# Performance work log

Measured on AMD Instinct MI355X. Metric: run time of the kernel, lower is better.

Reference implementation:

```python
import jax, jax.numpy as jnp
import numpy as np

B, NPATCH, PDIM, DIM, OUTD = 4, 1024, 768, 512, 512
DIN, DSTATE, DTRANK, KCONV, NBLK = 2 * DIM, 16, DIM // 16, 4, 2


def _ln(x, w, b, eps=1e-5):
    m = jnp.mean(x, -1, keepdims=True)
    v = jnp.var(x, -1, keepdims=True)
    return (x - m) * jax.lax.rsqrt(v + eps) * w + b


def _mamba_block(x, ln_w, ln_b, in_W, conv_w, conv_b, xproj_W, dt_W, dt_b, A_log, Dp, out_W):
    # x: [b, L, dim]
    b, L, _ = x.shape
    xn = _ln(x, ln_w, ln_b)
    xz = xn @ in_W                                # [b, L, 2*DIN]
    u, z = jnp.split(xz, 2, axis=-1)              # each [b, L, DIN]
    # causal depthwise conv over time
    uc = jnp.transpose(u, (0, 2, 1))              # [b, DIN, L]
    uc = jax.lax.conv_general_dilated(
        uc, conv_w[:, None, :], window_strides=(1,), padding=((KCONV - 1, 0),),
        feature_group_count=DIN)
    uc = uc + conv_b[None, :, None]
    u = jax.nn.silu(jnp.transpose(uc, (0, 2, 1)))  # [b, L, DIN]
    x_dbl = u @ xproj_W                            # [b, L, DTRANK+2*DSTATE]
    dt, Bm, Cm = jnp.split(x_dbl, [DTRANK, DTRANK + DSTATE], axis=-1)
    delta = jax.nn.softplus(dt @ dt_W + dt_b)      # [b, L, DIN]
    A = -jnp.exp(A_log)                            # [DIN, DSTATE]
    dA = jnp.exp(delta[..., None] * A)             # [b, L, DIN, DSTATE]
    dBu = delta[..., None] * Bm[:, :, None, :] * u[..., None]  # [b, L, DIN, DSTATE]
    # selective scan over time
    def step(h, inp):
        dA_t, dBu_t, C_t = inp                     # [b,DIN,DSTATE],[b,DIN,DSTATE],[b,DSTATE]
        h = dA_t * h + dBu_t
        y = jnp.einsum('bdn,bn->bd', h, C_t)
        return h, y
    h0 = jnp.zeros((b, DIN, DSTATE), x.dtype)
    _, ys = jax.lax.scan(step, h0, (jnp.swapaxes(dA, 0, 1), jnp.swapaxes(dBu, 0, 1), jnp.swapaxes(Cm, 0, 1)))
    y = jnp.swapaxes(ys, 0, 1) + u * Dp            # [b, L, DIN]
    y = y * jax.nn.silu(z)
    return x + y @ out_W                           # residual


def setup_inputs() -> dict:
    key = jax.random.key(0)
    ks = iter(jax.random.split(key, 40))
    rn = lambda shape, s=0.02: jax.random.normal(next(ks), shape, jnp.float32) * s
    d = {
        'img': jax.random.normal(next(ks), (B, NPATCH, PDIM), jnp.float32),
        'patch_W': rn((PDIM, DIM)), 'patch_b': jnp.zeros((DIM,), jnp.float32),
        'pos_emb': rn((1, NPATCH + 1, DIM), 1.0), 'cls_tok': rn((1, 1, DIM), 1.0),
        'blk_ln_w': jnp.ones((NBLK, DIM)), 'blk_ln_b': jnp.zeros((NBLK, DIM)),
        'blk_in_W': rn((NBLK, DIM, 2 * DIN)),
        'blk_conv_w': rn((NBLK, DIN, KCONV), 0.1), 'blk_conv_b': jnp.zeros((NBLK, DIN)),
        'blk_xproj_W': rn((NBLK, DIN, DTRANK + 2 * DSTATE)),
        'blk_dt_W': rn((NBLK, DTRANK, DIN), 0.1), 'blk_dt_b': jnp.full((NBLK, DIN), -4.0),
        'blk_A_log': jnp.tile(jnp.log(jnp.arange(1, DSTATE + 1, dtype=jnp.float32))[None, None, :], (NBLK, DIN, 1)),
        'blk_D': jnp.ones((NBLK, DIN)),
        'blk_out_W': rn((NBLK, DIN, DIM)),
        'sl1_W': rn((DIM, OUTD)), 'sl1_b': jnp.zeros((OUTD,)),
        'sl1_lnw': jnp.ones((OUTD,)), 'sl1_lnb': jnp.zeros((OUTD,)),
        'sl2_W': rn((OUTD, OUTD)), 'sl2_b': jnp.zeros((OUTD,)),
        'sl2_lnw': jnp.ones((OUTD,)), 'sl2_lnb': jnp.zeros((OUTD,)),
        'lat_lnw': jnp.ones((OUTD,)), 'lat_lnb': jnp.zeros((OUTD,)),
    }
    return d


def reference(img, patch_W, patch_b, pos_emb, cls_tok,
              blk_ln_w, blk_ln_b, blk_in_W, blk_conv_w, blk_conv_b,
              blk_xproj_W, blk_dt_W, blk_dt_b, blk_A_log, blk_D, blk_out_W,
              sl1_W, sl1_b, sl1_lnw, sl1_lnb, sl2_W, sl2_b, sl2_lnw, sl2_lnb,
              lat_lnw, lat_lnb):
    x = img @ patch_W + patch_b                       # [b, n, dim]
    b, n, _ = x.shape
    cls = jnp.broadcast_to(cls_tok, (b, 1, DIM))
    x = jnp.concatenate([cls, x], axis=1) + pos_emb[:, :n + 1]
    for i in range(NBLK):
        x = _mamba_block(x, blk_ln_w[i], blk_ln_b[i], blk_in_W[i], blk_conv_w[i],
                         blk_conv_b[i], blk_xproj_W[i], blk_dt_W[i], blk_dt_b[i],
                         blk_A_log[i], blk_D[i], blk_out_W[i])
    y = jax.nn.gelu(_ln(x @ sl1_W + sl1_b, sl1_lnw, sl1_lnb), approximate=False)
    a = jax.nn.gelu(_ln(y @ sl2_W + sl2_b, sl2_lnw, sl2_lnb), approximate=False)
    z = jax.nn.softmax(a, axis=1)                     # softmax over sequence dim
    pooled = jnp.sum(y * z, axis=1)                   # [b, outdim]
    return _ln(pooled, lat_lnw, lat_lnb)
```

## Files before the change

kernel.cpp:

```cpp
#include <hip/hip_runtime.h>
#include <cstdint>
#include <cstddef>

#define B_     4
#define NPATCH 1024
#define LSEQ   1025
#define PDIM   768
#define DIM    512
#define OUTD   512
#define DIN    1024
#define DSTATE 16
#define DTRANK 32
#define KCONV  4
#define NBLK   2
#define MROWS  (B_*LSEQ)
#define NSEG_SP 17

typedef unsigned short u16;
typedef __attribute__((ext_vector_type(8))) short bf16x8;
typedef __attribute__((ext_vector_type(4))) float f32x4;

__device__ __forceinline__ float sigmoidf_(float x){ return 1.f/(1.f+__expf(-x)); }
__device__ __forceinline__ float geluf_(float x){ return 0.5f*x*(1.f+erff(x*0.70710678118654752f)); }
__device__ __forceinline__ u16 f2bf(float x){
    uint32_t b = __float_as_uint(x);
    b += 0x7FFFu + ((b >> 16) & 1u);
    return (u16)(b >> 16);
}
template<int CTRL>
__device__ __forceinline__ float dppmov(float x){
    return __int_as_float(__builtin_amdgcn_update_dpp(0, __float_as_int(x), CTRL, 0xF, 0xF, true));
}
__device__ __forceinline__ float red16(float p){
    p += dppmov<0xB1>(p);
    p += dppmov<0x4E>(p);
    p += dppmov<0x141>(p);
    p += dppmov<0x140>(p);
    return p;
}
__device__ __forceinline__ void gload16(const void* g, void* l){
    __builtin_amdgcn_global_load_lds((const __attribute__((address_space(1))) void*)g,
                                     (__attribute__((address_space(3))) void*)l, 16, 0, 0);
}

template<int MF>
__global__ __launch_bounds__(256) void gemm_mfma(
    const u16* __restrict__ A, int lda,
    const u16* __restrict__ Wt,
    float* __restrict__ C, int ldc,
    int M, int N, int K,
    const float* __restrict__ bias,
    const float* __restrict__ addsrc,
    int act, u16* __restrict__ bf16out)
{
    __shared__ u16 lsA[MF*32*32];
    __shared__ u16 lsB[128*32];
    const int tid = threadIdx.x;
    const int wid = tid >> 6, lane = tid & 63;
    const int m0 = blockIdx.y * (MF*32), n0 = blockIdx.x * 128;
    const int wm = (wid>>1)*(MF*16), wn = (wid&1)*64;
    f32x4 acc[MF][4] = {};

    const char* Agp = (const char*)(A + (size_t)m0 * lda);
    const char* Bgp = (const char*)(Wt + (size_t)n0 * K);
    const int lrow = lane >> 2;
    const int lcb  = (lane & 3) * 16;

    for (int k0 = 0; k0 < K; k0 += 32) {
        {
            int ra = wid*(MF*8) + lrow;
            gload16(Agp + (size_t)ra*(lda*2) + k0*2 + lcb, &lsA[(wid*(MF*8))*32]);
            if constexpr (MF == 4) {
                gload16(Agp + (size_t)(ra+16)*(lda*2) + k0*2 + lcb, &lsA[(wid*(MF*8)+16)*32]);
            }
        }
        {
            int rb = wid*32 + lrow;
            gload16(Bgp + (size_t)rb*(K*2) + k0*2 + lcb, &lsB[(wid*32)*32]);
            gload16(Bgp + (size_t)(rb+16)*(K*2) + k0*2 + lcb, &lsB[(wid*32+16)*32]);
        }
        __syncthreads();
        bf16x8 af[MF], bfr[4];
        #pragma unroll
        for (int i = 0; i < MF; ++i)
            af[i] = *(const bf16x8*)&lsA[(wm + i*16 + (lane&15))*32 + (lane>>4)*8];
        #pragma unroll
        for (int j = 0; j < 4; ++j)
            bfr[j] = *(const bf16x8*)&lsB[(wn + j*16 + (lane&15))*32 + (lane>>4)*8];
        #pragma unroll
        for (int i = 0; i < MF; ++i)
            #pragma unroll
            for (int j = 0; j < 4; ++j)
                acc[i][j] = __builtin_amdgcn_mfma_f32_16x16x32_bf16(af[i], bfr[j], acc[i][j], 0, 0, 0);
        __syncthreads();
    }
    #pragma unroll
    for (int i = 0; i < MF; ++i) {
        #pragma unroll
        for (int j = 0; j < 4; ++j) {
            int col = n0 + wn + j*16 + (lane & 15);
            float bv = bias ? bias[col] : 0.f;
            #pragma unroll
            for (int r = 0; r < 4; ++r) {
                int row = m0 + wm + i*16 + (lane>>4)*4 + r;
                if (row < M) {
                    float v = acc[i][j][r] + bv;
                    if (addsrc) v += addsrc[(size_t)row*ldc + col];
                    if (act == 1) v = (v > 20.f) ? v : log1pf(__expf(v));
                    C[(size_t)row*ldc + col] = v;
                    if (bf16out) bf16out[(size_t)row*ldc + col] = f2bf(v);
                }
            }
        }
    }
}

__global__ __launch_bounds__(256) void xproj_gemm(
    const float* __restrict__ Au,
    const float* __restrict__ W,
    float* __restrict__ P)
{
    __shared__ float As[16][68];
    __shared__ float Bs[16][68];
    int tid = threadIdx.x;
    int tx = tid & 15, ty = tid >> 4;
    int m0 = blockIdx.x * 64;
    int kbase = blockIdx.y * 256;
    float acc[4][4] = {};
    for (int k0 = kbase; k0 < kbase + 256; k0 += 16) {
        {
            int r  = tid >> 2;
            int kq = (tid & 3) << 2;
            float4 va = make_float4(0.f,0.f,0.f,0.f);
            int gr = m0 + r;
            if (gr < MROWS) va = *reinterpret_cast<const float4*>(Au + (size_t)gr*DIN + k0 + kq);
            As[kq+0][r]=va.x; As[kq+1][r]=va.y; As[kq+2][r]=va.z; As[kq+3][r]=va.w;
        }
        {
            int kk = tid >> 4;
            int nq = (tid & 15) << 2;
            float4 vb = *reinterpret_cast<const float4*>(W + (size_t)(k0+kk)*64 + nq);
            Bs[kk][nq+0]=vb.x; Bs[kk][nq+1]=vb.y; Bs[kk][nq+2]=vb.z; Bs[kk][nq+3]=vb.w;
        }
        __syncthreads();
        #pragma unroll
        for (int k = 0; k < 16; ++k) {
            float a0=As[k][ty*4+0],a1=As[k][ty*4+1],a2=As[k][ty*4+2],a3=As[k][ty*4+3];
            float b0=Bs[k][tx*4+0],b1=Bs[k][tx*4+1],b2=Bs[k][tx*4+2],b3=Bs[k][tx*4+3];
            acc[0][0]=fmaf(a0,b0,acc[0][0]); acc[0][1]=fmaf(a0,b1,acc[0][1]);
            acc[0][2]=fmaf(a0,b2,acc[0][2]); acc[0][3]=fmaf(a0,b3,acc[0][3]);
            acc[1][0]=fmaf(a1,b0,acc[1][0]); acc[1][1]=fmaf(a1,b1,acc[1][1]);
            acc[1][2]=fmaf(a1,b2,acc[1][2]); acc[1][3]=fmaf(a1,b3,acc[1][3]);
            acc[2][0]=fmaf(a2,b0,acc[2][0]); acc[2][1]=fmaf(a2,b1,acc[2][1]);
            acc[2][2]=fmaf(a2,b2,acc[2][2]); acc[2][3]=fmaf(a2,b3,acc[2][3]);
            acc[3][0]=fmaf(a3,b0,acc[3][0]); acc[3][1]=fmaf(a3,b1,acc[3][1]);
            acc[3][2]=fmaf(a3,b2,acc[3][2]); acc[3][3]=fmaf(a3,b3,acc[3][3]);
        }
        __syncthreads();
    }
    float* Pp = P + (size_t)blockIdx.y * (MROWS*64);
    #pragma unroll
    for (int i = 0; i < 4; ++i) {
        int r = m0 + ty*4 + i;
        if (r >= MROWS) continue;
        #pragma unroll
        for (int j = 0; j < 4; ++j)
            Pp[(size_t)r*64 + tx*4 + j] = acc[i][j];
    }
}

__global__ __launch_bounds__(256) void xproj_reduce(
    const float* __restrict__ P, float* __restrict__ xdbl, u16* __restrict__ xdbl_bf)
{
    int idx = blockIdx.x*256 + threadIdx.x;
    float v = P[idx] + P[MROWS*64 + idx] + P[2*MROWS*64 + idx] + P[3*MROWS*64 + idx];
    xdbl[idx] = v;
    xdbl_bf[idx] = f2bf(v);
}

__device__ void tcast(const float* __restrict__ in, u16* __restrict__ outp,
                      int K, int N, int tix)
{
    __shared__ float tl[32][33];
    int ntn = N >> 5;
    int tk = tix / ntn, tn = tix - tk*ntn;
    int tid = threadIdx.x;
    int r = tid >> 3, c0 = (tid & 7) << 2;
    float4 v = *(const float4*)&in[(size_t)(tk*32 + r)*N + tn*32 + c0];
    tl[r][c0+0]=v.x; tl[r][c0+1]=v.y; tl[r][c0+2]=v.z; tl[r][c0+3]=v.w;
    __syncthreads();
    int nn = r, k0 = c0;
    uint32_t w0 = f2bf(tl[k0+0][nn]) | ((uint32_t)f2bf(tl[k0+1][nn]) << 16);
    uint32_t w1 = f2bf(tl[k0+2][nn]) | ((uint32_t)f2bf(tl[k0+3][nn]) << 16);
    uint2 o; o.x = w0; o.y = w1;
    *(uint2*)&outp[(size_t)(tn*32 + nn)*K + tk*32 + k0] = o;
}

__global__ __launch_bounds__(256) void prep_kernel(
    const float* __restrict__ img, const float* __restrict__ pW,
    const float* __restrict__ inW, const float* __restrict__ outW,
    const float* __restrict__ dtW, const float* __restrict__ s1W,
    const float* __restrict__ s2W,
    u16* imgb, u16* pWt, u16* inWt, u16* outWt, u16* dtWt, u16* s1t, u16* s2t)
{
    int b = blockIdx.x;
    if (b < 3072) {
        int idx = b*1024 + threadIdx.x*4;
        float4 v = *(const float4*)&img[idx];
        uint2 o;
        o.x = f2bf(v.x) | ((uint32_t)f2bf(v.y) << 16);
        o.y = f2bf(v.z) | ((uint32_t)f2bf(v.w) << 16);
        *(uint2*)&imgb[idx] = o;
        return;
    }
    b -= 3072;
    if (b < 384)  { tcast(pW, pWt, 768, 512, b); return; }
    b -= 384;
    if (b < 2048) { int blk=b>>10, t=b&1023; tcast(inW + (size_t)blk*512*2048, inWt + (size_t)blk*1048576, 512, 2048, t); return; }
    b -= 2048;
    if (b < 1024) { int blk=b>>9, t=b&511; tcast(outW + (size_t)blk*1024*512, outWt + (size_t)blk*524288, 1024, 512, t); return; }
    b -= 1024;
    if (b < 64)   { int blk=b>>5, t=b&31; tcast(dtW + (size_t)blk*32*1024, dtWt + (size_t)blk*32768, 32, 1024, t); return; }
    b -= 64;
    if (b < 256)  { tcast(s1W, s1t, 512, 512, b); return; }
    b -= 256;
    tcast(s2W, s2t, 512, 512, b);
}

__global__ __launch_bounds__(256) void assemble_x(
    const float* __restrict__ tmp, const float* __restrict__ cls,
    const float* __restrict__ pos, float* __restrict__ x)
{
    int idx = blockIdx.x*256 + threadIdx.x;
    int d = idx & 511;
    int r = idx >> 9;
    int l = r % LSEQ;
    int b = r / LSEQ;
    float v = (l == 0) ? cls[d] : tmp[((size_t)(b*NPATCH + l-1))*DIM + d];
    x[idx] = v + pos[(size_t)l*DIM + d];
}

__global__ __launch_bounds__(256) void ln_act(
    const float* __restrict__ in, const float* __restrict__ gw, const float* __restrict__ gb,
    float* __restrict__ f32out, u16* __restrict__ bf16out, int act)
{
    int row = blockIdx.x;
    const float* p = in + (size_t)row * 512;
    int t = threadIdx.x;
    float v0 = p[t], v1 = p[t + 256];
    float s = v0 + v1, q = v0*v0 + v1*v1;
    #pragma unroll
    for (int o = 32; o; o >>= 1) { s += __shfl_xor(s, o); q += __shfl_xor(q, o); }
    __shared__ float ls[4], lq[4];
    int w = t >> 6;
    if ((t & 63) == 0) { ls[w] = s; lq[w] = q; }
    __syncthreads();
    s = ls[0]+ls[1]+ls[2]+ls[3];
    q = lq[0]+lq[1]+lq[2]+lq[3];
    float mean = s * (1.f/512.f);
    float var  = q * (1.f/512.f) - mean*mean;
    float inv  = rsqrtf(var + 1e-5f);
    float o0 = (v0-mean)*inv*gw[t]     + gb[t];
    float o1 = (v1-mean)*inv*gw[t+256] + gb[t+256];
    if (act == 2) { o0 = geluf_(o0); o1 = geluf_(o1); }
    if (f32out)  { f32out[(size_t)row*512 + t] = o0; f32out[(size_t)row*512 + t + 256] = o1; }
    if (bf16out) { bf16out[(size_t)row*512 + t] = f2bf(o0); bf16out[(size_t)row*512 + t + 256] = f2bf(o1); }
}

__global__ __launch_bounds__(256) void conv_silu(
    const float* __restrict__ xz, const float* __restrict__ cw,
    const float* __restrict__ cb, float* __restrict__ uo)
{
    int idx = blockIdx.x*256 + threadIdx.x;
    int dq = idx & 255;
    int r  = idx >> 8;
    int b = r / LSEQ, l = r - b*LSEQ;
    int d0 = dq << 2;
    float4 w0 = *(const float4*)&cw[(d0+0)*4];
    float4 w1 = *(const float4*)&cw[(d0+1)*4];
    float4 w2 = *(const float4*)&cw[(d0+2)*4];
    float4 w3 = *(const float4*)&cw[(d0+3)*4];
    float4 acc = *(const float4*)&cb[d0];
    const float* wv0 = &w0.x; const float* wv1 = &w1.x;
    const float* wv2 = &w2.x; const float* wv3 = &w3.x;
    #pragma unroll
    for (int k = 0; k < KCONV; ++k) {
        int ls = l - (KCONV-1) + k;
        if (ls >= 0) {
            float4 v = *(const float4*)&xz[((size_t)(b*LSEQ + ls))*2048 + d0];
            acc.x = fmaf(wv0[k], v.x, acc.x);
            acc.y = fmaf(wv1[k], v.y, acc.y);
            acc.z = fmaf(wv2[k], v.z, acc.z);
            acc.w = fmaf(wv3[k], v.w, acc.w);
        }
    }
    acc.x *= sigmoidf_(acc.x);
    acc.y *= sigmoidf_(acc.y);
    acc.z *= sigmoidf_(acc.z);
    acc.w *= sigmoidf_(acc.w);
    *(float4*)&uo[(size_t)r*DIN + d0] = acc;
}

__global__ __launch_bounds__(256) void scan_phase1(
    const float* __restrict__ delta, const float* __restrict__ u,
    const float* __restrict__ xdbl,  const float* __restrict__ A_log,
    float* __restrict__ Aseg, float* __restrict__ Hseg)
{
    const int dg = blockIdx.x, b = blockIdx.y, s = blockIdx.z;
    const int tid = threadIdx.x;
    const int n = tid & 15, dl = tid >> 4;
    const int d0 = dg*16, d = d0 + dl;
    const float Adn = -__expf(A_log[(size_t)d*DSTATE + n]);
    float ap = 1.f, h = 0.f;
    __shared__ float sD[16][16], sU[16][16], sB[16][16];
    const size_t base = (size_t)b*LSEQ + (size_t)s*128;
    for (int c0 = 0; c0 < 128; c0 += 16) {
        __syncthreads();
        {
            int tr = tid >> 4, tc = tid & 15;
            size_t row = base + c0 + tr;
            sD[tr][tc] = delta[row*DIN + d0+tc];
            sU[tr][tc] = u[row*DIN + d0+tc];
            sB[tr][tc] = xdbl[row*64 + DTRANK + tc];
        }
        __syncthreads();
        #pragma unroll
        for (int t = 0; t < 16; ++t) {
            float dv = sD[t][dl], uv = sU[t][dl], Bv = sB[t][n];
            float dA = __expf(dv * Adn);
            ap *= dA;
            h = fmaf(dA, h, dv*uv*Bv);
        }
    }
    int dn = d*DSTATE + n;
    Aseg[((size_t)b*7 + s)*16384 + dn] = ap;
    Hseg[((size_t)b*8 + s)*16384 + dn] = h;
}

__global__ __launch_bounds__(256) void scan_mid(
    float* __restrict__ Hseg, const float* __restrict__ Aseg)
{
    int idx = blockIdx.x*256 + threadIdx.x;
    int b = idx >> 14, dn = idx & 16383;
    float prev = 0.f;
    #pragma unroll
    for (int s = 0; s < 7; ++s) {
        size_t offH = ((size_t)b*8 + s)*16384 + dn;
        float a  = Aseg[((size_t)b*7 + s)*16384 + dn];
        float hs = Hseg[offH];
        Hseg[offH] = prev;
        prev = fmaf(a, prev, hs);
    }
    Hseg[((size_t)b*8 + 7)*16384 + dn] = prev;
}

__global__ __launch_bounds__(256) void scan_phase2(
    const float* __restrict__ delta, const float* __restrict__ u,
    const float* __restrict__ xdbl,  const float* __restrict__ xz,
    const float* __restrict__ A_log, const float* __restrict__ Dp,
    const float* __restrict__ H0, u16* __restrict__ yb)
{
    const int dg = blockIdx.x, b = blockIdx.y, s = blockIdx.z;
    const int tid = threadIdx.x;
    const int n = tid & 15, dl = tid >> 4;
    const int d0 = dg*16, d = d0 + dl;
    const float Adn = -__expf(A_log[(size_t)d*DSTATE + n]);
    const float Dd = Dp[d];
    float h = H0[((size_t)b*8 + s)*16384 + d*DSTATE + n];
    __shared__ float sD[16][16], sU[16][16], sZ[16][16], sB[16][16], sC[16][16];
    __shared__ u16 sY[16][16];
    const size_t base = (size_t)b*LSEQ + (size_t)s*128;
    for (int c0 = 0; c0 < 128; c0 += 16) {
        __syncthreads();
        {
            int tr = tid >> 4, tc = tid & 15;
            size_t row = base + c0 + tr;
            sD[tr][tc] = delta[row*DIN + d0+tc];
            sU[tr][tc] = u[row*DIN + d0+tc];
            sZ[tr][tc] = xz[row*2048 + DIN + d0+tc];
            sB[tr][tc] = xdbl[row*64 + DTRANK + tc];
            sC[tr][tc] = xdbl[row*64 + DTRANK + DSTATE + tc];
        }
        __syncthreads();
        #pragma unroll
        for (int t = 0; t < 16; ++t) {
            float dv = sD[t][dl], uv = sU[t][dl], Bv = sB[t][n], Cv = sC[t][n];
            float dA = __expf(dv * Adn);
            h = fmaf(dA, h, dv*uv*Bv);
            float p = red16(h * Cv);
            if (n == 0) {
                float zv = sZ[t][dl];
                sY[t][dl] = f2bf((p + uv*Dd) * (zv * sigmoidf_(zv)));
            }
        }
        __syncthreads();
        {
            int tr = tid >> 4, tc = tid & 15;
            yb[(base + c0 + tr)*DIN + d0 + tc] = sY[tr][tc];
        }
    }
    if (s == 7) {
        size_t row = (size_t)b*LSEQ + 1024;
        float dv = delta[row*DIN + d];
        float uv = u[row*DIN + d];
        float zv = xz[row*2048 + DIN + d];
        float Bv = xdbl[row*64 + DTRANK + n];
        float Cv = xdbl[row*64 + DTRANK + DSTATE + n];
        float dA = __expf(dv * Adn);
        h = fmaf(dA, h, dv*uv*Bv);
        float p = red16(h * Cv);
        if (n == 0)
            yb[row*DIN + d] = f2bf((p + uv*Dd) * (zv * sigmoidf_(zv)));
    }
}

__global__ __launch_bounds__(256) void softpool_seg(
    const float* __restrict__ a, const float* __restrict__ yh,
    float* __restrict__ pm, float* __restrict__ ps, float* __restrict__ pp)
{
    int b   = blockIdx.y;
    int seg = blockIdx.z;
    int jj = threadIdx.x & 63;
    int j  = blockIdx.x * 64 + jj;
    int li = threadIdx.x >> 6;
    int lbeg = seg * 64;
    int lend = min(lbeg + 64, LSEQ);
    float m = -3.0e38f, s = 0.f, p = 0.f;
    for (int l = lbeg + li; l < lend; l += 4) {
        size_t off = ((size_t)(b*LSEQ + l))*OUTD + j;
        float av = a[off], yv = yh[off];
        float mn = fmaxf(m, av);
        float sc = __expf(m - mn);
        float e  = __expf(av - mn);
        s = s*sc + e;
        p = p*sc + yv*e;
        m = mn;
    }
    __shared__ float sm[4][64], ss[4][64], sp[4][64];
    sm[li][jj] = m; ss[li][jj] = s; sp[li][jj] = p;
    __syncthreads();
    if (li == 0) {
        #pragma unroll
        for (int k2 = 1; k2 < 4; ++k2) {
            float m2 = sm[k2][jj], s2 = ss[k2][jj], p2 = sp[k2][jj];
            float M2 = fmaxf(m, m2);
            float c1 = __expf(m - M2), c2 = __expf(m2 - M2);
            s = s*c1 + s2*c2;
            p = p*c1 + p2*c2;
            m = M2;
        }
        int o = ((seg*B_ + b)*OUTD) + j;
        pm[o] = m; ps[o] = s; pp[o] = p;
    }
}

__global__ __launch_bounds__(256) void softpool_combine(
    const float* __restrict__ pm, const float* __restrict__ ps,
    const float* __restrict__ pp, float* __restrict__ pooled)
{
    int idx = blockIdx.x*256 + threadIdx.x;
    int b = idx >> 9, j = idx & 511;
    float m = -3.0e38f, s = 0.f, p = 0.f;
    #pragma unroll
    for (int seg = 0; seg < NSEG_SP; ++seg) {
        int o = ((seg*B_ + b)*OUTD) + j;
        float m2 = pm[o], s2 = ps[o], p2 = pp[o];
        float M2 = fmaxf(m, m2);
        float c1 = __expf(m - M2), c2 = __expf(m2 - M2);
        s = s*c1 + s2*c2;
        p = p*c1 + p2*c2;
        m = M2;
    }
    pooled[(size_t)b*OUTD + j] = p / s;
}

extern "C" void kernel_launch(void* const* d_in, const int* in_sizes, int n_in,
                              void* d_out, int out_size, void* d_ws, size_t ws_size,
                              hipStream_t stream) {
    const float* img     = (const float*)d_in[0];
    const float* patch_W = (const float*)d_in[1];
    const float* patch_b = (const float*)d_in[2];
    const float* pos_emb = (const float*)d_in[3];
    const float* cls_tok = (const float*)d_in[4];
    const float* ln_w    = (const float*)d_in[5];
    const float* ln_b    = (const float*)d_in[6];
    const float* in_W    = (const float*)d_in[7];
    const float* conv_w  = (const float*)d_in[8];
    const float* conv_b  = (const float*)d_in[9];
    const float* xproj_W = (const float*)d_in[10];
    const float* dt_W    = (const float*)d_in[11];
    const float* dt_b    = (const float*)d_in[12];
    const float* A_log   = (const float*)d_in[13];
    const float* Dp      = (const float*)d_in[14];
    const float* out_W   = (const float*)d_in[15];
    const float* sl1_W   = (const float*)d_in[16];
    const float* sl1_b   = (const float*)d_in[17];
    const float* sl1_lnw = (const float*)d_in[18];
    const float* sl1_lnb = (const float*)d_in[19];
    const float* sl2_W   = (const float*)d_in[20];
    const float* sl2_b   = (const float*)d_in[21];
    const float* sl2_lnw = (const float*)d_in[22];
    const float* sl2_lnb = (const float*)d_in[23];
    const float* lat_lnw = (const float*)d_in[24];
    const float* lat_lnb = (const float*)d_in[25];
    float* out = (float*)d_out;
    float* ws  = (float*)d_ws;

    float* x     = ws + 0;
    float* xz    = ws + 2099200;
    float* u     = ws + 10496000;
    float* xdbl  = ws + 14694400;
    float* delta = ws + 14956800;
    u16* ub      = (u16*)(ws + 19155200);
    u16* regA    = ub + 0;
    u16* regB    = ub + 4325376;
    u16* xdbl_bf = ub + 6488064;
    u16* pWt     = ub + 6758400;
    u16* inWt    = ub + 7151616;
    u16* outWt   = ub + 9248768;
    u16* dtWt    = ub + 10297344;
    u16* s1t     = ub + 10362880;
    u16* s2t     = ub + 10625024;

    float* yh     = xz;
    float* t2     = xz + 2099200;
    float* a      = u;
    float* pooled = xdbl;
    float* spm    = xdbl + 8192;
    float* sps    = spm + 34816;
    float* spp    = sps + 34816;
    float* t1     = delta;
    float* segH   = (float*)regB;
    float* segA   = segH + 524288;
    float* xprojP = delta;

    prep_kernel<<<7104, 256, 0, stream>>>(img, patch_W, in_W, out_W, dt_W, sl1_W, sl2_W,
                                          regA, pWt, inWt, outWt, dtWt, s1t, s2t);

    gemm_mfma<2><<<dim3(512/128, 4096/64), 256, 0, stream>>>(
        regA, PDIM, pWt, delta, DIM, 4096, DIM, PDIM, patch_b, nullptr, 0, nullptr);
    assemble_x<<<(MROWS*DIM)/256, 256, 0, stream>>>(delta, cls_tok, pos_emb, x);

    for (int i = 0; i < NBLK; ++i) {
        ln_act<<<MROWS, 256, 0, stream>>>(x, ln_w + i*DIM, ln_b + i*DIM,
                                          nullptr, regB, 0);
        gemm_mfma<4><<<dim3(2048/128, 33), 256, 0, stream>>>(
            regB, DIM, inWt + (size_t)i*1048576, xz, 2*DIN,
            MROWS, 2*DIN, DIM, nullptr, nullptr, 0, nullptr);
        conv_silu<<<MROWS, 256, 0, stream>>>(
            xz, conv_w + i*DIN*KCONV, conv_b + i*DIN, u);
        xproj_gemm<<<dim3(65, 4), 256, 0, stream>>>(
            u, xproj_W + (size_t)i*DIN*64, xprojP);
        xproj_reduce<<<1025, 256, 0, stream>>>(xprojP, xdbl, xdbl_bf);
        gemm_mfma<2><<<dim3(1024/128, 65), 256, 0, stream>>>(
            xdbl_bf, 64, dtWt + (size_t)i*32768, delta, DIN,
            MROWS, DIN, DTRANK, dt_b + i*DIN, nullptr, 1, nullptr);
        scan_phase1<<<dim3(64, 4, 7), 256, 0, stream>>>(
            delta, u, xdbl, A_log + (size_t)i*DIN*DSTATE, segA, segH);
        scan_mid<<<256, 256, 0, stream>>>(segH, segA);
        scan_phase2<<<dim3(64, 4, 8), 256, 0, stream>>>(
            delta, u, xdbl, xz, A_log + (size_t)i*DIN*DSTATE, Dp + i*DIN,
            segH, regA);
        gemm_mfma<2><<<dim3(512/128, 65), 256, 0, stream>>>(
            regA, DIN, outWt + (size_t)i*524288, x, DIM,
            MROWS, DIM, DIN, nullptr, x, 0, (i == NBLK-1) ? regB : nullptr);
    }

    gemm_mfma<2><<<dim3(512/128, 65), 256, 0, stream>>>(
        regB, DIM, s1t, t1, OUTD, MROWS, OUTD, DIM, sl1_b, nullptr, 0, nullptr);
    ln_act<<<MROWS, 256, 0, stream>>>(t1, sl1_lnw, sl1_lnb, yh, regA, 2);
    gemm_mfma<2><<<dim3(512/128, 65), 256, 0, stream>>>(
        regA, OUTD, s2t, t2, OUTD, MROWS, OUTD, OUTD, sl2_b, nullptr, 0, nullptr);
    ln_act<<<MROWS, 256, 0, stream>>>(t2, sl2_lnw, sl2_lnb, a, nullptr, 2);
    softpool_seg<<<dim3(OUTD/64, B_, NSEG_SP), 256, 0, stream>>>(a, yh, spm, sps, spp);
    softpool_combine<<<8, 256, 0, stream>>>(spm, sps, spp, pooled);
    ln_act<<<B_, 256, 0, stream>>>(pooled, lat_lnw, lat_lnb, out, nullptr, 0);
}
```

Baseline: 632.6 us.

## Swizzle GEMM LDS layout and vectorize scan shared-memory reads with transposed tiles

```diff
diff --git a/kernel.cpp b/kernel.cpp
--- a/kernel.cpp
+++ b/kernel.cpp
@@ -64,7 +64,9 @@
     const char* Agp = (const char*)(A + (size_t)m0 * lda);
     const char* Bgp = (const char*)(Wt + (size_t)n0 * K);
     const int lrow = lane >> 2;
-    const int lcb  = (lane & 3) * 16;
+    const int lcb  = (((lane & 3) ^ ((lane >> 3) & 3))) * 16;
+    const int rsw  = ((lane & 15) >> 1) & 3;
+    const int acol = ((lane >> 4) ^ rsw) * 8;
 
     for (int k0 = 0; k0 < K; k0 += 32) {
         {
@@ -83,10 +85,10 @@
         bf16x8 af[MF], bfr[4];
         #pragma unroll
         for (int i = 0; i < MF; ++i)
-            af[i] = *(const bf16x8*)&lsA[(wm + i*16 + (lane&15))*32 + (lane>>4)*8];
+            af[i] = *(const bf16x8*)&lsA[(wm + i*16 + (lane&15))*32 + acol];
         #pragma unroll
         for (int j = 0; j < 4; ++j)
-            bfr[j] = *(const bf16x8*)&lsB[(wn + j*16 + (lane&15))*32 + (lane>>4)*8];
+            bfr[j] = *(const bf16x8*)&lsB[(wn + j*16 + (lane&15))*32 + acol];
         #pragma unroll
         for (int i = 0; i < MF; ++i)
             #pragma unroll
@@ -310,30 +312,41 @@
     const int tid = threadIdx.x;
     const int n = tid & 15, dl = tid >> 4;
     const int d0 = dg*16, d = d0 + dl;
-    const float Adn = -__expf(A_log[(size_t)d*DSTATE + n]);
-    float ap = 1.f, h = 0.f;
-    __shared__ float sD[16][16], sU[16][16], sB[16][16];
+    const float Adn2 = -__expf(A_log[(size_t)d*DSTATE + n]) * 1.44269504f;
+    float sdv = 0.f, h = 0.f;
+    __shared__ float sD[16][20], sU[16][20], sB[16][20];
+    const int tr = tid >> 4, tc = tid & 15;
     const size_t base = (size_t)b*LSEQ + (size_t)s*128;
     for (int c0 = 0; c0 < 128; c0 += 16) {
         __syncthreads();
         {
-            int tr = tid >> 4, tc = tid & 15;
             size_t row = base + c0 + tr;
-            sD[tr][tc] = delta[row*DIN + d0+tc];
-            sU[tr][tc] = u[row*DIN + d0+tc];
-            sB[tr][tc] = xdbl[row*64 + DTRANK + tc];
-        }
-        __syncthreads();
-        #pragma unroll
-        for (int t = 0; t < 16; ++t) {
-            float dv = sD[t][dl], uv = sU[t][dl], Bv = sB[t][n];
-            float dA = __expf(dv * Adn);
-            ap *= dA;
-            h = fmaf(dA, h, dv*uv*Bv);
+            sD[tc][tr] = delta[row*DIN + d0 + tc];
+            sU[tc][tr] = u[row*DIN + d0 + tc];
+            sB[tc][tr] = xdbl[row*64 + DTRANK + tc];
+        }
+        __syncthreads();
+        #pragma unroll
+        for (int hf = 0; hf < 2; ++hf) {
+            f32x4 vD0 = *(const f32x4*)&sD[dl][hf*8];
+            f32x4 vD1 = *(const f32x4*)&sD[dl][hf*8+4];
+            f32x4 vU0 = *(const f32x4*)&sU[dl][hf*8];
+            f32x4 vU1 = *(const f32x4*)&sU[dl][hf*8+4];
+            f32x4 vB0 = *(const f32x4*)&sB[n][hf*8];
+            f32x4 vB1 = *(const f32x4*)&sB[n][hf*8+4];
+            #pragma unroll
+            for (int t = 0; t < 8; ++t) {
+                float dv = (t<4) ? vD0[t&3] : vD1[t&3];
+                float uv = (t<4) ? vU0[t&3] : vU1[t&3];
+                float Bv = (t<4) ? vB0[t&3] : vB1[t&3];
+                sdv += dv;
+                float dA = __builtin_exp2f(dv * Adn2);
+                h = fmaf(dA, h, dv*uv*Bv);
+            }
         }
     }
     int dn = d*DSTATE + n;
-    Aseg[((size_t)b*7 + s)*16384 + dn] = ap;
+    Aseg[((size_t)b*7 + s)*16384 + dn] = __builtin_exp2f(Adn2 * sdv);
     Hseg[((size_t)b*8 + s)*16384 + dn] = h;
 }
 
@@ -364,40 +377,56 @@
     const int tid = threadIdx.x;
     const int n = tid & 15, dl = tid >> 4;
     const int d0 = dg*16, d = d0 + dl;
-    const float Adn = -__expf(A_log[(size_t)d*DSTATE + n]);
+    const float Adn2 = -__expf(A_log[(size_t)d*DSTATE + n]) * 1.44269504f;
     const float Dd = Dp[d];
     float h = H0[((size_t)b*8 + s)*16384 + d*DSTATE + n];
-    __shared__ float sD[16][16], sU[16][16], sZ[16][16], sB[16][16], sC[16][16];
-    __shared__ u16 sY[16][16];
+    __shared__ float sD[16][20], sU[16][20], sZ[16][20], sB[16][20], sC[16][20];
+    __shared__ u16 sY[16][20];
+    const int tr = tid >> 4, tc = tid & 15;
     const size_t base = (size_t)b*LSEQ + (size_t)s*128;
     for (int c0 = 0; c0 < 128; c0 += 16) {
         __syncthreads();
         {
-            int tr = tid >> 4, tc = tid & 15;
             size_t row = base + c0 + tr;
-            sD[tr][tc] = delta[row*DIN + d0+tc];
-            sU[tr][tc] = u[row*DIN + d0+tc];
-            sZ[tr][tc] = xz[row*2048 + DIN + d0+tc];
-            sB[tr][tc] = xdbl[row*64 + DTRANK + tc];
-            sC[tr][tc] = xdbl[row*64 + DTRANK + DSTATE + tc];
-        }
-        __syncthreads();
-        #pragma unroll
-        for (int t = 0; t < 16; ++t) {
-            float dv = sD[t][dl], uv = sU[t][dl], Bv = sB[t][n], Cv = sC[t][n];
-            float dA = __expf(dv * Adn);
-            h = fmaf(dA, h, dv*uv*Bv);
-            float p = red16(h * Cv);
-            if (n == 0) {
-                float zv = sZ[t][dl];
-                sY[t][dl] = f2bf((p + uv*Dd) * (zv * sigmoidf_(zv)));
+            sD[tc][tr] = delta[row*DIN + d0 + tc];
+            sU[tc][tr] = u[row*DIN + d0 + tc];
+            sZ[tc][tr] = xz[row*2048 + DIN + d0 + tc];
+            sB[tc][tr] = xdbl[row*64 + DTRANK + tc];
+            sC[tc][tr] = xdbl[row*64 + DTRANK + DSTATE + tc];
+        }
+        __syncthreads();
+        float py = 0.f;
+        #pragma unroll
+        for (int hf = 0; hf < 2; ++hf) {
+            f32x4 vD0 = *(const f32x4*)&sD[dl][hf*8];
+            f32x4 vD1 = *(const f32x4*)&sD[dl][hf*8+4];
+            f32x4 vU0 = *(const f32x4*)&sU[dl][hf*8];
+            f32x4 vU1 = *(const f32x4*)&sU[dl][hf*8+4];
+            f32x4 vB0 = *(const f32x4*)&sB[n][hf*8];
+            f32x4 vB1 = *(const f32x4*)&sB[n][hf*8+4];
+            f32x4 vC0 = *(const f32x4*)&sC[n][hf*8];
+            f32x4 vC1 = *(const f32x4*)&sC[n][hf*8+4];
+            #pragma unroll
+            for (int t = 0; t < 8; ++t) {
+                float dv = (t<4) ? vD0[t&3] : vD1[t&3];
+                float uv = (t<4) ? vU0[t&3] : vU1[t&3];
+                float Bv = (t<4) ? vB0[t&3] : vB1[t&3];
+                float Cv = (t<4) ? vC0[t&3] : vC1[t&3];
+                float dA = __builtin_exp2f(dv * Adn2);
+                h = fmaf(dA, h, dv*uv*Bv);
+                float pr = red16(h * Cv);
+                int tt = hf*8 + t;
+                py = (n == tt) ? pr : py;
             }
         }
-        __syncthreads();
         {
-            int tr = tid >> 4, tc = tid & 15;
-            yb[(base + c0 + tr)*DIN + d0 + tc] = sY[tr][tc];
-        }
+            float uv = sU[dl][n];
+            float zv = sZ[dl][n];
+            float yv = (py + uv*Dd) * (zv * sigmoidf_(zv));
+            sY[n][dl] = f2bf(yv);
+        }
+        __syncthreads();
+        yb[(base + c0 + tr)*DIN + d0 + tc] = sY[tr][tc];
     }
     if (s == 7) {
         size_t row = (size_t)b*LSEQ + 1024;
@@ -406,7 +435,7 @@
         float zv = xz[row*2048 + DIN + d];
         float Bv = xdbl[row*64 + DTRANK + n];
         float Cv = xdbl[row*64 + DTRANK + DSTATE + n];
-        float dA = __expf(dv * Adn);
+        float dA = __builtin_exp2f(dv * Adn2);
         h = fmaf(dA, h, dv*uv*Bv);
         float p = red16(h * Cv);
         if (n == 0)
```

Result: no change. 632.1 us (-0.1%).
